# Kernel tuning notes

Measured on AMD Instinct MI355X. Metric: run time of the kernel, lower is better.

## Reference

```python
import jax, jax.numpy as jnp
import numpy as np

B, T, D, E, V = 16, 256, 512, 512, 32000  # batch, seqlen, embed_dim, encoder_embed_dim, vocab


def setup_inputs() -> dict:
    key = jax.random.key(0)
    ks = jax.random.split(key, 13)
    s = 0.05
    return {
        "prev_output_tokens": jax.random.randint(ks[0], (B, T), 0, V),
        "encoder_out": jax.random.normal(ks[1], (B, E), jnp.float32),
        "embed": jax.random.normal(ks[2], (V, D), jnp.float32) * s,
        "W_ih0": jax.random.normal(ks[3], (4 * D, E + D), jnp.float32) * s,
        "W_hh0": jax.random.normal(ks[4], (4 * D, D), jnp.float32) * s,
        "b_ih0": jax.random.normal(ks[5], (4 * D,), jnp.float32) * s,
        "b_hh0": jax.random.normal(ks[6], (4 * D,), jnp.float32) * s,
        "W_ih1": jax.random.normal(ks[7], (4 * D, D), jnp.float32) * s,
        "W_hh1": jax.random.normal(ks[8], (4 * D, D), jnp.float32) * s,
        "b_ih1": jax.random.normal(ks[9], (4 * D,), jnp.float32) * s,
        "b_hh1": jax.random.normal(ks[10], (4 * D,), jnp.float32) * s,
        "W_out": jax.random.normal(ks[11], (V, D), jnp.float32) * s,
        "b_out": jax.random.normal(ks[12], (V,), jnp.float32) * s,
    }


def _lstm_cell(x, h, c, W_ih, W_hh, b_ih, b_hh):
    # torch.nn.LSTMCell gate order: i, f, g, o
    gates = x @ W_ih.T + b_ih + h @ W_hh.T + b_hh
    i, f, g, o = jnp.split(gates, 4, axis=-1)
    c_new = jax.nn.sigmoid(f) * c + jax.nn.sigmoid(i) * jnp.tanh(g)
    h_new = jax.nn.sigmoid(o) * jnp.tanh(c_new)
    return h_new, c_new


def reference(prev_output_tokens, encoder_out, embed, W_ih0, W_hh0, b_ih0, b_hh0,
              W_ih1, W_hh1, b_ih1, b_hh1, W_out, b_out):
    # padding_idx=0 -> row 0 of the embedding table is zero
    embed = embed.at[0].set(0.0)
    x = embed[prev_output_tokens]          # [B, T, D]  (dropout: eval mode -> identity)
    x = jnp.swapaxes(x, 0, 1)              # [T, B, D]
    bsz = x.shape[1]
    h0 = jnp.zeros((bsz, W_hh0.shape[1]), x.dtype)
    c0, h1, c1 = h0, h0, h0

    def step(carry, x_t):
        h0, c0, h1, c1 = carry
        inp = jnp.concatenate([x_t, encoder_out], axis=1)   # [B, D+E]
        h0, c0 = _lstm_cell(inp, h0, c0, W_ih0, W_hh0, b_ih0, b_hh0)
        h1, c1 = _lstm_cell(h0, h1, c1, W_ih1, W_hh1, b_ih1, b_hh1)
        return (h0, c0, h1, c1), h1

    _, outs = jax.lax.scan(step, (h0, c0, h1, c1), x)       # outs: [T, B, D]
    outs = jnp.swapaxes(outs, 0, 1)                          # [B, T, D]
    return outs @ W_out.T + b_out                            # [B, T, V]
```

## Files before the change

### kernel.cpp

```cpp
#include <hip/hip_runtime.h>
#include <hip/hip_bf16.h>
#include <math.h>

#define BB 16
#define TT 256
#define DD 512
#define EE 512
#define VV 32000
#define G4 2048

typedef __attribute__((ext_vector_type(4))) float f32x4;
typedef __attribute__((ext_vector_type(8))) short bf16x8;

union frag_u { unsigned long long u[2]; bf16x8 v; };

#define SENTMASK 0x4000400040004000ULL

__device__ __forceinline__ unsigned short f2bf(float x) {
    unsigned u = __float_as_uint(x);
    unsigned r = (u + 0x7FFFu + ((u >> 16) & 1u)) >> 16;
    return (unsigned short)r;
}

__device__ __forceinline__ float sigmoidf_(float x) { return 1.0f / (1.0f + expf(-x)); }

__global__ __launch_bounds__(256) void k_gather(const int* __restrict__ tok,
        const float* __restrict__ embed, unsigned short* __restrict__ Xb) {
    int m = blockIdx.x;
    int tk = tok[m];
    const float* src = embed + (size_t)tk * DD;
    int i = threadIdx.x * 2;
    float vx = 0.f, vy = 0.f;
    if (tk != 0) { float2 v = *(const float2*)&src[i]; vx = v.x; vy = v.y; }
    ushort2 o; o.x = f2bf(vx); o.y = f2bf(vy);
    *(ushort2*)&Xb[(size_t)m * DD + i] = o;
}

__global__ __launch_bounds__(256) void k_cvt(const float* __restrict__ in,
        unsigned short* __restrict__ out, int n4) {
    int i = blockIdx.x * 256 + threadIdx.x;
    if (i >= n4) return;
    float4 v = ((const float4*)in)[i];
    ushort4 o; o.x = f2bf(v.x); o.y = f2bf(v.y); o.z = f2bf(v.z); o.w = f2bf(v.w);
    ((ushort4*)out)[i] = o;
}

__global__ __launch_bounds__(256) void k_cvt_wih0x(const float* __restrict__ Wih0,
        unsigned short* __restrict__ out) {
    int i = blockIdx.x * 256 + threadIdx.x;
    int j = i >> 7;
    int k4 = (i & 127) << 2;
    float4 v = *(const float4*)&Wih0[(size_t)j * (EE + DD) + k4];
    ushort4 o; o.x = f2bf(v.x); o.y = f2bf(v.y); o.z = f2bf(v.z); o.w = f2bf(v.w);
    *(ushort4*)&out[(size_t)j * DD + k4] = o;
}

__global__ __launch_bounds__(256) void k_encterm(const float* __restrict__ enc,
        const float* __restrict__ Wih0, const float* __restrict__ bih0,
        const float* __restrict__ bhh0, float* __restrict__ et) {
    int b = blockIdx.x >> 3, jc = blockIdx.x & 7;
    int tid = threadIdx.x, lane = tid & 63, w = tid >> 6;
    __shared__ float es[EE];
    if (tid < EE / 4) *(float4*)&es[tid * 4] = *(const float4*)&enc[b * EE + tid * 4];
    __syncthreads();
    float4 e0 = *(const float4*)&es[lane * 4];
    float4 e1 = *(const float4*)&es[256 + lane * 4];
    for (int o = 0; o < 64; ++o) {
        int j = jc * 256 + w * 64 + o;
        const float4* Wr = (const float4*)&Wih0[(size_t)j * (EE + DD) + DD];
        float4 w0 = Wr[lane], w1 = Wr[64 + lane];
        float s = w0.x*e0.x + w0.y*e0.y + w0.z*e0.z + w0.w*e0.w
                + w1.x*e1.x + w1.y*e1.y + w1.z*e1.z + w1.w*e1.w;
        #pragma unroll
        for (int off = 32; off; off >>= 1) s += __shfl_xor(s, off);
        if (lane == 0) et[b * G4 + j] = s + bih0[j] + bhh0[j];
    }
}

template<int EPI>
__global__ __launch_bounds__(256) void k_gemm_bt(
        const unsigned short* __restrict__ A, const unsigned short* __restrict__ Bm,
        float* __restrict__ C, const float* __restrict__ extra,
        int M, int N, int K) {
    __shared__ __align__(16) unsigned short Alds[128 * 32];
    __shared__ __align__(16) unsigned short Blds[128 * 32];
    int tid = threadIdx.x, lane = tid & 63, w = tid >> 6;
    int wr = w >> 1, wc = w & 1;
    int m0 = blockIdx.x * 128, n0 = blockIdx.y * 128;
    f32x4 acc[4][4];
    #pragma unroll
    for (int i = 0; i < 4; i++)
        #pragma unroll
        for (int j = 0; j < 4; j++) acc[i][j] = (f32x4)0.f;

    const char* Abase = (const char*)A;
    const char* Bbase = (const char*)Bm;
    for (int ks = 0; ks < K; ks += 32) {
        #pragma unroll
        for (int c = 0; c < 2; ++c) {
            int f = (tid + c * 256) * 16;
            int row = f >> 6;
            int inb = f & 63;
            const char* gA = Abase + (((size_t)(m0 + row) * K + ks) * 2 + inb);
            __builtin_amdgcn_global_load_lds(
                (const __attribute__((address_space(1))) void*)gA,
                (__attribute__((address_space(3))) void*)((char*)Alds + f), 16, 0, 0);
            const char* gB = Bbase + (((size_t)(n0 + row) * K + ks) * 2 + inb);
            __builtin_amdgcn_global_load_lds(
                (const __attribute__((address_space(1))) void*)gB,
                (__attribute__((address_space(3))) void*)((char*)Blds + f), 16, 0, 0);
        }
        __syncthreads();
        bf16x8 af[4], bfr[4];
        int r = lane & 15, ko = (lane >> 4) * 8;
        #pragma unroll
        for (int mi = 0; mi < 4; ++mi)
            af[mi] = *(const bf16x8*)&Alds[(wr * 64 + mi * 16 + r) * 32 + ko];
        #pragma unroll
        for (int ni = 0; ni < 4; ++ni)
            bfr[ni] = *(const bf16x8*)&Blds[(wc * 64 + ni * 16 + r) * 32 + ko];
        #pragma unroll
        for (int mi = 0; mi < 4; ++mi)
            #pragma unroll
            for (int ni = 0; ni < 4; ++ni)
                acc[mi][ni] = __builtin_amdgcn_mfma_f32_16x16x32_bf16(af[mi], bfr[ni], acc[mi][ni], 0, 0, 0);
        __syncthreads();
    }
    int cr = (lane >> 4) * 4, cc = lane & 15;
    #pragma unroll
    for (int mi = 0; mi < 4; ++mi) {
        #pragma unroll
        for (int ni = 0; ni < 4; ++ni) {
            int col = n0 + wc * 64 + ni * 16 + cc;
            #pragma unroll
            for (int rr = 0; rr < 4; ++rr) {
                int rowg = m0 + wr * 64 + mi * 16 + cr + rr;
                float v = acc[mi][ni][rr];
                if (EPI == 0) v += extra[(rowg >> 8) * G4 + col];
                else          v += extra[col];
                C[(size_t)rowg * N + col] = v;
            }
        }
    }
}

__device__ __forceinline__ void poll16(const unsigned long long* row, int q,
        unsigned long long* ax, unsigned long long* ay) {
    for (;;) {
        unsigned long long bad = 0;
        #pragma unroll
        for (int kt = 0; kt < 16; ++kt) {
            ax[kt] = __hip_atomic_load(row + kt * 8 + q * 2,
                                       __ATOMIC_RELAXED, __HIP_MEMORY_SCOPE_AGENT);
            ay[kt] = __hip_atomic_load(row + kt * 8 + q * 2 + 1,
                                       __ATOMIC_RELAXED, __HIP_MEMORY_SCOPE_AGENT);
            bad |= (ax[kt] | ay[kt]) & SENTMASK;
        }
        if (!__any(bad != 0)) break;
    }
}

__global__ __launch_bounds__(64) void k_recur(
        const float* __restrict__ Gx,
        const float* __restrict__ Whh0,
        const float* __restrict__ Wih1, const float* __restrict__ Whh1,
        const float* __restrict__ bih1, const float* __restrict__ bhh1,
        unsigned short* h0hist, unsigned short* outsb,
        const unsigned short* zbuf) {
    __shared__ __align__(16) unsigned short wfrag[4 * 32 * 512];
    __shared__ __align__(8)  unsigned short houts[16 * 16];
    const int l = threadIdx.x;
    const int bid = blockIdx.x;
    const int role = bid >> 5;
    const int blk = bid & 31;
    const int d0 = blk * 16;
    const int r16 = l & 15;
    const int q = l >> 4;
    const int ksub = q * 8;
    const int b0 = q * 4;
    const int srow = l >> 2;
    const int sseg = l & 3;

    const int nkt = role ? 32 : 16;
    for (int tile = 0; tile < 4; ++tile) {
        int j = tile * 512 + d0 + r16;
        for (int kt = 0; kt < nkt; ++kt) {
            const float* src;
            if (role == 0)    src = Whh0 + (size_t)j * DD + kt * 32 + ksub;
            else if (kt < 16) src = Wih1 + (size_t)j * DD + kt * 32 + ksub;
            else              src = Whh1 + (size_t)j * DD + (kt - 16) * 32 + ksub;
            float4 x = *(const float4*)src;
            float4 y = *(const float4*)(src + 4);
            bf16x8 w;
            w[0] = f2bf(x.x); w[1] = f2bf(x.y); w[2] = f2bf(x.z); w[3] = f2bf(x.w);
            w[4] = f2bf(y.x); w[5] = f2bf(y.y); w[6] = f2bf(y.z); w[7] = f2bf(y.w);
            *(bf16x8*)&wfrag[((tile * 32 + kt) * 64 + l) * 8] = w;
        }
    }
    __syncthreads();

    float cst[4] = {0.f, 0.f, 0.f, 0.f};
    unsigned long long ax[16], ay[16];

    if (role == 0) {
        for (int t = 0; t < TT; ++t) {
            float gx[4][4];
            #pragma unroll
            for (int ni = 0; ni < 4; ++ni)
                #pragma unroll
                for (int rr = 0; rr < 4; ++rr)
                    gx[ni][rr] = Gx[((size_t)(b0 + rr) * TT + t) * G4 + ni * 512 + d0 + r16];

            const unsigned long long* hrow =
                (const unsigned long long*)(h0hist + (size_t)t * (BB * DD) + r16 * DD);
            poll16(hrow, q, ax, ay);

            f32x4 acc[4];
            #pragma unroll
            for (int ni = 0; ni < 4; ++ni) acc[ni] = (f32x4)0.f;
            #pragma unroll
            for (int kt = 0; kt < 16; ++kt) {
                frag_u f; f.u[0] = ax[kt]; f.u[1] = ay[kt];
                #pragma unroll
                for (int ni = 0; ni < 4; ++ni) {
                    bf16x8 wf = *(const bf16x8*)&wfrag[((ni * 32 + kt) * 64 + l) * 8];
                    acc[ni] = __builtin_amdgcn_mfma_f32_16x16x32_bf16(f.v, wf, acc[ni], 0, 0, 0);
                }
            }
            #pragma unroll
            for (int rr = 0; rr < 4; ++rr) {
                float gi = acc[0][rr] + gx[0][rr], gf = acc[1][rr] + gx[1][rr];
                float gg = acc[2][rr] + gx[2][rr], go = acc[3][rr] + gx[3][rr];
                float cn = sigmoidf_(gf) * cst[rr] + sigmoidf_(gi) * tanhf(gg);
                float hn = sigmoidf_(go) * tanhf(cn);
                cst[rr] = cn;
                houts[(b0 + rr) * 16 + r16] = f2bf(hn);
            }
            asm volatile("" ::: "memory");
            {
                const unsigned short* hp = &houts[srow * 16 + sseg * 4];
                unsigned long long w8 =  (unsigned long long)hp[0]
                                      | ((unsigned long long)hp[1] << 16)
                                      | ((unsigned long long)hp[2] << 32)
                                      | ((unsigned long long)hp[3] << 48);
                __hip_atomic_store(
                    (unsigned long long*)(h0hist + (size_t)(t + 1) * (BB * DD) + srow * DD + d0 + sseg * 4),
                    w8, __ATOMIC_RELAXED, __HIP_MEMORY_SCOPE_AGENT);
            }
        }
    } else {
        float bin[4];
        #pragma unroll
        for (int ni = 0; ni < 4; ++ni)
            bin[ni] = bih1[ni * 512 + d0 + r16] + bhh1[ni * 512 + d0 + r16];
        for (int t = 0; t < TT; ++t) {
            const unsigned long long* xrow =
                (const unsigned long long*)(h0hist + (size_t)(t + 1) * (BB * DD) + r16 * DD);
            poll16(xrow, q, ax, ay);

            f32x4 acc[4];
            #pragma unroll
            for (int ni = 0; ni < 4; ++ni)
                acc[ni] = (f32x4){bin[ni], bin[ni], bin[ni], bin[ni]};
            #pragma unroll
            for (int kt = 0; kt < 16; ++kt) {
                frag_u f; f.u[0] = ax[kt]; f.u[1] = ay[kt];
                #pragma unroll
                for (int ni = 0; ni < 4; ++ni) {
                    bf16x8 wf = *(const bf16x8*)&wfrag[((ni * 32 + kt) * 64 + l) * 8];
                    acc[ni] = __builtin_amdgcn_mfma_f32_16x16x32_bf16(f.v, wf, acc[ni], 0, 0, 0);
                }
            }
            const unsigned long long* hrow = (t == 0)
                ? (const unsigned long long*)(zbuf + r16 * DD)
                : (const unsigned long long*)(outsb + ((size_t)r16 * TT + (t - 1)) * DD);
            poll16(hrow, q, ax, ay);
            #pragma unroll
            for (int kt = 0; kt < 16; ++kt) {
                frag_u f; f.u[0] = ax[kt]; f.u[1] = ay[kt];
                #pragma unroll
                for (int ni = 0; ni < 4; ++ni) {
                    bf16x8 wf = *(const bf16x8*)&wfrag[((ni * 32 + 16 + kt) * 64 + l) * 8];
                    acc[ni] = __builtin_amdgcn_mfma_f32_16x16x32_bf16(f.v, wf, acc[ni], 0, 0, 0);
                }
            }
            #pragma unroll
            for (int rr = 0; rr < 4; ++rr) {
                float gi = acc[0][rr], gf = acc[1][rr], gg = acc[2][rr], go = acc[3][rr];
                float cn = sigmoidf_(gf) * cst[rr] + sigmoidf_(gi) * tanhf(gg);
                float hn = sigmoidf_(go) * tanhf(cn);
                cst[rr] = cn;
                houts[(b0 + rr) * 16 + r16] = f2bf(hn);
            }
            asm volatile("" ::: "memory");
            {
                const unsigned short* hp = &houts[srow * 16 + sseg * 4];
                unsigned long long w8 =  (unsigned long long)hp[0]
                                      | ((unsigned long long)hp[1] << 16)
                                      | ((unsigned long long)hp[2] << 32)
                                      | ((unsigned long long)hp[3] << 48);
                __hip_atomic_store(
                    (unsigned long long*)(outsb + ((size_t)srow * TT + t) * DD + d0 + sseg * 4),
                    w8, __ATOMIC_RELAXED, __HIP_MEMORY_SCOPE_AGENT);
            }
        }
    }
}

extern "C" void kernel_launch(void* const* d_in, const int* in_sizes, int n_in,
                              void* d_out, int out_size, void* d_ws, size_t ws_size,
                              hipStream_t stream) {
    const int*   tok   = (const int*)  d_in[0];
    const float* enc   = (const float*)d_in[1];
    const float* embed = (const float*)d_in[2];
    const float* Wih0  = (const float*)d_in[3];
    const float* Whh0  = (const float*)d_in[4];
    const float* bih0  = (const float*)d_in[5];
    const float* bhh0  = (const float*)d_in[6];
    const float* Wih1  = (const float*)d_in[7];
    const float* Whh1  = (const float*)d_in[8];
    const float* bih1  = (const float*)d_in[9];
    const float* bhh1  = (const float*)d_in[10];
    const float* Wout  = (const float*)d_in[11];
    const float* bout  = (const float*)d_in[12];
    float* out = (float*)d_out;

    char* ws = (char*)d_ws;
    size_t off = 0;
    auto alloc = [&](size_t bytes) -> char* {
        char* p = ws + off; off += (bytes + 255) & ~(size_t)255; return p;
    };
    unsigned short* Xb     = (unsigned short*)alloc((size_t)BB * TT * DD * 2);
    unsigned short* Wih0xb = (unsigned short*)alloc((size_t)G4 * DD * 2);
    unsigned short* Woutb  = (unsigned short*)alloc((size_t)VV * DD * 2);
    float*          et     = (float*)alloc((size_t)BB * G4 * sizeof(float));
    float*          Gx     = (float*)alloc((size_t)BB * TT * G4 * sizeof(float));
    unsigned short* outsb  = (unsigned short*)alloc((size_t)BB * TT * DD * 2);
    unsigned short* h0hist = (unsigned short*)alloc((size_t)(TT + 1) * BB * DD * 2);
    unsigned short* zbuf   = (unsigned short*)alloc((size_t)BB * DD * 2);

    hipMemsetAsync(h0hist, 0, (size_t)BB * DD * 2, stream);
    hipMemsetAsync(h0hist + (size_t)BB * DD, 0xFF, (size_t)TT * BB * DD * 2, stream);
    hipMemsetAsync(outsb, 0xFF, (size_t)BB * TT * DD * 2, stream);
    hipMemsetAsync(zbuf, 0, (size_t)BB * DD * 2, stream);

    k_gather<<<BB * TT, 256, 0, stream>>>(tok, embed, Xb);
    k_cvt<<<(VV * DD / 4 + 255) / 256, 256, 0, stream>>>(Wout, Woutb, VV * DD / 4);
    k_cvt_wih0x<<<(G4 * DD / 4) / 256, 256, 0, stream>>>(Wih0, Wih0xb);
    k_encterm<<<BB * 8, 256, 0, stream>>>(enc, Wih0, bih0, bhh0, et);

    dim3 g1(BB * TT / 128, G4 / 128);
    k_gemm_bt<0><<<g1, 256, 0, stream>>>(Xb, Wih0xb, Gx, et, BB * TT, G4, DD);

    k_recur<<<64, 64, 0, stream>>>(Gx, Whh0, Wih1, Whh1, bih1, bhh1,
                                   h0hist, outsb, zbuf);

    dim3 g2(BB * TT / 128, VV / 128);
    k_gemm_bt<1><<<g2, 256, 0, stream>>>(outsb, Woutb, out, bout, BB * TT, VV, DD);
}
```

Measured before the change: 1.853 ms.

## Consume recurrent hidden-state chunks incrementally as they arrive instead of full-row polling

Replaces the all-or-nothing poll of a full 512-wide hidden row with per-k-chunk readiness tracking. Each 32-wide chunk whose sentinel bits are clear is fed to the MFMAs immediately, and only the missing chunks are reloaded. Layer 1 now polls its x-input row and its own previous h row together, so work on either can start as soon as parts arrive. This overlaps cross-block communication latency with matrix math, at the cost of more branching, more registers (extra bx/by arrays) and divergence-free but serialized __any checks per chunk.

```diff
diff --git a/kernel.cpp b/kernel.cpp
--- a/kernel.cpp
+++ b/kernel.cpp
@@ -141,22 +141,6 @@
                 C[(size_t)rowg * N + col] = v;
             }
         }
-    }
-}
-
-__device__ __forceinline__ void poll16(const unsigned long long* row, int q,
-        unsigned long long* ax, unsigned long long* ay) {
-    for (;;) {
-        unsigned long long bad = 0;
-        #pragma unroll
-        for (int kt = 0; kt < 16; ++kt) {
-            ax[kt] = __hip_atomic_load(row + kt * 8 + q * 2,
-                                       __ATOMIC_RELAXED, __HIP_MEMORY_SCOPE_AGENT);
-            ay[kt] = __hip_atomic_load(row + kt * 8 + q * 2 + 1,
-                                       __ATOMIC_RELAXED, __HIP_MEMORY_SCOPE_AGENT);
-            bad |= (ax[kt] | ay[kt]) & SENTMASK;
-        }
-        if (!__any(bad != 0)) break;
     }
 }
 
@@ -200,9 +184,9 @@
     __syncthreads();
 
     float cst[4] = {0.f, 0.f, 0.f, 0.f};
-    unsigned long long ax[16], ay[16];
 
     if (role == 0) {
+        unsigned long long ax[16], ay[16];
         for (int t = 0; t < TT; ++t) {
             float gx[4][4];
             #pragma unroll
@@ -213,20 +197,35 @@
 
             const unsigned long long* hrow =
                 (const unsigned long long*)(h0hist + (size_t)t * (BB * DD) + r16 * DD);
-            poll16(hrow, q, ax, ay);
 
             f32x4 acc[4];
             #pragma unroll
             for (int ni = 0; ni < 4; ++ni) acc[ni] = (f32x4)0.f;
-            #pragma unroll
-            for (int kt = 0; kt < 16; ++kt) {
-                frag_u f; f.u[0] = ax[kt]; f.u[1] = ay[kt];
-                #pragma unroll
-                for (int ni = 0; ni < 4; ++ni) {
-                    bf16x8 wf = *(const bf16x8*)&wfrag[((ni * 32 + kt) * 64 + l) * 8];
-                    acc[ni] = __builtin_amdgcn_mfma_f32_16x16x32_bf16(f.v, wf, acc[ni], 0, 0, 0);
-                }
-            }
+
+            unsigned pend = 0xFFFFu;
+            while (pend) {
+                unsigned p = pend;
+                #pragma unroll
+                for (int kt = 0; kt < 16; ++kt) if (p & (1u << kt)) {
+                    ax[kt] = __hip_atomic_load(hrow + kt * 8 + q * 2,
+                                               __ATOMIC_RELAXED, __HIP_MEMORY_SCOPE_AGENT);
+                    ay[kt] = __hip_atomic_load(hrow + kt * 8 + q * 2 + 1,
+                                               __ATOMIC_RELAXED, __HIP_MEMORY_SCOPE_AGENT);
+                }
+                #pragma unroll
+                for (int kt = 0; kt < 16; ++kt) if (p & (1u << kt)) {
+                    if (!__any(((ax[kt] | ay[kt]) & SENTMASK) != 0)) {
+                        frag_u f; f.u[0] = ax[kt]; f.u[1] = ay[kt];
+                        #pragma unroll
+                        for (int ni = 0; ni < 4; ++ni) {
+                            bf16x8 wf = *(const bf16x8*)&wfrag[((ni * 32 + kt) * 64 + l) * 8];
+                            acc[ni] = __builtin_amdgcn_mfma_f32_16x16x32_bf16(f.v, wf, acc[ni], 0, 0, 0);
+                        }
+                        pend &= ~(1u << kt);
+                    }
+                }
+            }
+
             #pragma unroll
             for (int rr = 0; rr < 4; ++rr) {
                 float gi = acc[0][rr] + gx[0][rr], gf = acc[1][rr] + gx[1][rr];
@@ -249,6 +248,7 @@
             }
         }
     } else {
+        unsigned long long ax[16], ay[16], bx[16], by[16];
         float bin[4];
         #pragma unroll
         for (int ni = 0; ni < 4; ++ni)
@@ -256,34 +256,58 @@
         for (int t = 0; t < TT; ++t) {
             const unsigned long long* xrow =
                 (const unsigned long long*)(h0hist + (size_t)(t + 1) * (BB * DD) + r16 * DD);
-            poll16(xrow, q, ax, ay);
-
-            f32x4 acc[4];
-            #pragma unroll
-            for (int ni = 0; ni < 4; ++ni)
-                acc[ni] = (f32x4){bin[ni], bin[ni], bin[ni], bin[ni]};
-            #pragma unroll
-            for (int kt = 0; kt < 16; ++kt) {
-                frag_u f; f.u[0] = ax[kt]; f.u[1] = ay[kt];
-                #pragma unroll
-                for (int ni = 0; ni < 4; ++ni) {
-                    bf16x8 wf = *(const bf16x8*)&wfrag[((ni * 32 + kt) * 64 + l) * 8];
-                    acc[ni] = __builtin_amdgcn_mfma_f32_16x16x32_bf16(f.v, wf, acc[ni], 0, 0, 0);
-                }
-            }
             const unsigned long long* hrow = (t == 0)
                 ? (const unsigned long long*)(zbuf + r16 * DD)
                 : (const unsigned long long*)(outsb + ((size_t)r16 * TT + (t - 1)) * DD);
-            poll16(hrow, q, ax, ay);
-            #pragma unroll
-            for (int kt = 0; kt < 16; ++kt) {
-                frag_u f; f.u[0] = ax[kt]; f.u[1] = ay[kt];
-                #pragma unroll
-                for (int ni = 0; ni < 4; ++ni) {
-                    bf16x8 wf = *(const bf16x8*)&wfrag[((ni * 32 + 16 + kt) * 64 + l) * 8];
-                    acc[ni] = __builtin_amdgcn_mfma_f32_16x16x32_bf16(f.v, wf, acc[ni], 0, 0, 0);
-                }
-            }
+
+            f32x4 acc[4];
+            #pragma unroll
+            for (int ni = 0; ni < 4; ++ni)
+                acc[ni] = (f32x4){bin[ni], bin[ni], bin[ni], bin[ni]};
+
+            unsigned pendx = 0xFFFFu, pendh = 0xFFFFu;
+            while (pendx | pendh) {
+                unsigned px = pendx, ph = pendh;
+                #pragma unroll
+                for (int kt = 0; kt < 16; ++kt) if (px & (1u << kt)) {
+                    ax[kt] = __hip_atomic_load(xrow + kt * 8 + q * 2,
+                                               __ATOMIC_RELAXED, __HIP_MEMORY_SCOPE_AGENT);
+                    ay[kt] = __hip_atomic_load(xrow + kt * 8 + q * 2 + 1,
+                                               __ATOMIC_RELAXED, __HIP_MEMORY_SCOPE_AGENT);
+                }
+                #pragma unroll
+                for (int kt = 0; kt < 16; ++kt) if (ph & (1u << kt)) {
+                    bx[kt] = __hip_atomic_load(hrow + kt * 8 + q * 2,
+                                               __ATOMIC_RELAXED, __HIP_MEMORY_SCOPE_AGENT);
+                    by[kt] = __hip_atomic_load(hrow + kt * 8 + q * 2 + 1,
+                                               __ATOMIC_RELAXED, __HIP_MEMORY_SCOPE_AGENT);
+                }
+                #pragma unroll
+                for (int kt = 0; kt < 16; ++kt) if (ph & (1u << kt)) {
+                    if (!__any(((bx[kt] | by[kt]) & SENTMASK) != 0)) {
+                        frag_u f; f.u[0] = bx[kt]; f.u[1] = by[kt];
+                        #pragma unroll
+                        for (int ni = 0; ni < 4; ++ni) {
+                            bf16x8 wf = *(const bf16x8*)&wfrag[((ni * 32 + 16 + kt) * 64 + l) * 8];
+                            acc[ni] = __builtin_amdgcn_mfma_f32_16x16x32_bf16(f.v, wf, acc[ni], 0, 0, 0);
+                        }
+                        pendh &= ~(1u << kt);
+                    }
+                }
+                #pragma unroll
+                for (int kt = 0; kt < 16; ++kt) if (px & (1u << kt)) {
+                    if (!__any(((ax[kt] | ay[kt]) & SENTMASK) != 0)) {
+                        frag_u f; f.u[0] = ax[kt]; f.u[1] = ay[kt];
+                        #pragma unroll
+                        for (int ni = 0; ni < 4; ++ni) {
+                            bf16x8 wf = *(const bf16x8*)&wfrag[((ni * 32 + kt) * 64 + l) * 8];
+                            acc[ni] = __builtin_amdgcn_mfma_f32_16x16x32_bf16(f.v, wf, acc[ni], 0, 0, 0);
+                        }
+                        pendx &= ~(1u << kt);
+                    }
+                }
+            }
+
             #pragma unroll
             for (int rr = 0; rr < 4; ++rr) {
                 float gi = acc[0][rr], gf = acc[1][rr], gg = acc[2][rr], go = acc[3][rr];
```

Measured after the change: 2.680 ms. 1.45x slower.
